# Kernel tuning notes

Measured on AMD Instinct MI355X. Metric: run time of the kernel, lower is better.

Reference implementation:

```python
import jax, jax.numpy as jnp
import numpy as np

V = 33
EPS = 1e-5
PAD = 4  # (temporal_k=9 - 1) // 2
BONES = [(0,1),(1,2),(2,3),(3,7),(0,4),(4,5),(5,6),(6,8),(9,10),(11,12),(11,13),(13,15),(15,17),(15,19),(15,21),(17,19),(12,14),(14,16),(16,18),(16,20),(16,22),(18,20),(11,23),(12,24),(23,24),(23,25),(24,26),(25,27),(26,28),(27,29),(28,30),(29,31),(30,32),(27,31),(28,32)]


def _build_A():
    A = np.zeros((V, V), np.float32)
    for a, b in BONES:
        A[a, b] = 1.0
        A[b, a] = 1.0
    A = A + np.eye(V, dtype=np.float32)
    dis = np.diag(A.sum(1) ** -0.5)
    return jnp.asarray((dis @ A @ dis).astype(np.float32))


def _bn(x, g, b, m, v):
    # inference-mode BatchNorm2d over channel axis 1 of (B,C,T,V)
    inv = g / jnp.sqrt(v + EPS)
    return x * inv[None, :, None, None] + (b - m * inv)[None, :, None, None]


def _block(x, A, pw, pb, g1, b1, m1, v1, tw, tb, g2, b2, m2, v2, rw=None, rb=None):
    # residual branch (1x1 conv if channels change, else identity)
    r = x if rw is None else jnp.einsum('bctv,oc->botv', x, rw) + rb[None, :, None, None]
    # spatial GCN: per-joint 1x1 conv then adjacency mix along joints
    y = jnp.einsum('bctv,oc->botv', x, pw) + pb[None, :, None, None]
    y = jnp.einsum('bctv,vw->bctw', y, A)
    y = jax.nn.relu(_bn(y, g1, b1, m1, v1))
    # temporal conv: kernel (9,1), same padding along T
    y = jax.lax.conv_general_dilated(y, tw, (1, 1), ((PAD, PAD), (0, 0)),
                                     dimension_numbers=('NCHW', 'OIHW', 'NCHW'))
    y = _bn(y + tb[None, :, None, None], g2, b2, m2, v2)
    # Dropout2d is identity in inference mode
    return jax.nn.relu(y + r)


def setup_inputs() -> dict:
    key = jax.random.key(0)
    ks = iter(jax.random.split(key, 80))
    B, C, T, NC = 64, 6, 256, 100
    chans = [6, 32, 64, 64]
    inp = {'x': jax.random.normal(next(ks), (B, C, T, V), jnp.float32),
           'A': _build_A()}

    def add_bn(p, n):
        inp[p + '_g'] = jax.random.uniform(next(ks), (n,), jnp.float32) + 0.5
        inp[p + '_b'] = jax.random.normal(next(ks), (n,), jnp.float32) * 0.1
        inp[p + '_m'] = jax.random.normal(next(ks), (n,), jnp.float32) * 0.1
        inp[p + '_v'] = jax.random.uniform(next(ks), (n,), jnp.float32) + 0.5

    add_bn('bn_in', C * V)
    for i in range(3):
        ci, co = chans[i], chans[i + 1]
        p = 'b%d' % i
        inp[p + '_proj_w'] = jax.random.normal(next(ks), (co, ci), jnp.float32) / np.sqrt(ci).astype(np.float32)
        inp[p + '_proj_b'] = jnp.zeros((co,), jnp.float32)
        add_bn(p + '_bn1', co)
        inp[p + '_tcn_w'] = jax.random.normal(next(ks), (co, co, 9, 1), jnp.float32) / np.sqrt(co * 9).astype(np.float32)
        inp[p + '_tcn_b'] = jnp.zeros((co,), jnp.float32)
        add_bn(p + '_bn2', co)
        if ci != co:
            inp[p + '_res_w'] = jax.random.normal(next(ks), (co, ci), jnp.float32) / np.sqrt(ci).astype(np.float32)
            inp[p + '_res_b'] = jnp.zeros((co,), jnp.float32)
    inp['fc_w'] = jax.random.normal(next(ks), (NC, 64), jnp.float32) * 0.1
    inp['fc_b'] = jnp.zeros((NC,), jnp.float32)
    return inp


def reference(x, A, bn_in_g, bn_in_b, bn_in_m, bn_in_v,
              b0_proj_w, b0_proj_b, b0_bn1_g, b0_bn1_b, b0_bn1_m, b0_bn1_v,
              b0_tcn_w, b0_tcn_b, b0_bn2_g, b0_bn2_b, b0_bn2_m, b0_bn2_v,
              b0_res_w, b0_res_b,
              b1_proj_w, b1_proj_b, b1_bn1_g, b1_bn1_b, b1_bn1_m, b1_bn1_v,
              b1_tcn_w, b1_tcn_b, b1_bn2_g, b1_bn2_b, b1_bn2_m, b1_bn2_v,
              b1_res_w, b1_res_b,
              b2_proj_w, b2_proj_b, b2_bn1_g, b2_bn1_b, b2_bn1_m, b2_bn1_v,
              b2_tcn_w, b2_tcn_b, b2_bn2_g, b2_bn2_b, b2_bn2_m, b2_bn2_v,
              fc_w, fc_b):
    B, C, T, _ = x.shape
    # input BN over C*V channels: torch views as (B, C*V, T) with channel c*V+v
    inv = (bn_in_g / jnp.sqrt(bn_in_v + EPS)).reshape(C, V)
    shift = (bn_in_b - bn_in_m * bn_in_g / jnp.sqrt(bn_in_v + EPS)).reshape(C, V)
    h = x * inv[None, :, None, :] + shift[None, :, None, :]
    h = _block(h, A, b0_proj_w, b0_proj_b, b0_bn1_g, b0_bn1_b, b0_bn1_m, b0_bn1_v,
               b0_tcn_w, b0_tcn_b, b0_bn2_g, b0_bn2_b, b0_bn2_m, b0_bn2_v, b0_res_w, b0_res_b)
    h = _block(h, A, b1_proj_w, b1_proj_b, b1_bn1_g, b1_bn1_b, b1_bn1_m, b1_bn1_v,
               b1_tcn_w, b1_tcn_b, b1_bn2_g, b1_bn2_b, b1_bn2_m, b1_bn2_v, b1_res_w, b1_res_b)
    h = _block(h, A, b2_proj_w, b2_proj_b, b2_bn1_g, b2_bn1_b, b2_bn1_m, b2_bn1_v,
               b2_tcn_w, b2_tcn_b, b2_bn2_g, b2_bn2_b, b2_bn2_m, b2_bn2_v)
    feat = h.mean(axis=(2, 3))  # global avg pool over T, V -> (B, 64)
    return feat @ fc_w.T + fc_b
```

## Files before the change

kernel.cpp:

```cpp
#include <hip/hip_runtime.h>


typedef short bf16s;
using v8s = __attribute__((ext_vector_type(8))) short;
using v4f = __attribute__((ext_vector_type(4))) float;

#define TV 8448
#define NB 64
#define EPSBN 1e-5f

__device__ __forceinline__ float b2f(short s) {
  unsigned u = ((unsigned)(unsigned short)s) << 16;
  return __builtin_bit_cast(float, u);
}
__device__ __forceinline__ short f2b(float f) {
  unsigned u = __builtin_bit_cast(unsigned, f);
  u += 0x7FFFu + ((u >> 16) & 1u);
  return (short)(u >> 16);
}

constexpr int NOFF[34] = {0,3,6,9,12,15,18,21,23,25,27,29,33,37,40,43,48,53,
                          56,59,62,65,67,69,73,77,80,83,87,91,94,97,100,103};
constexpr int NBR[103] = {
  0,1,4,    0,1,2,    1,2,3,    2,3,7,    0,4,5,    4,5,6,    5,6,8,
  3,7,      6,8,      9,10,     9,10,
  11,12,13,23,  11,12,14,24,  11,13,15,  12,14,16,
  13,15,17,19,21,  14,16,18,20,22,
  15,17,19,  16,18,20,  15,17,19,  16,18,20,  15,21,  16,22,
  11,23,24,25,  12,23,24,26,  23,25,27,  24,26,28,
  25,27,29,31,  26,28,30,32,  27,29,31,  28,30,32,  27,29,31,  28,30,32};

constexpr int P_A     = 0;
constexpr int P_INV0  = 1089;
constexpr int P_BIAS0 = 1287;
constexpr int P_PB0   = 1485;
constexpr int P_PB1   = 1517;
constexpr int P_PB2   = 1581;
constexpr int P_I1_0  = 1645;  constexpr int P_B1_0 = 1677;
constexpr int P_I2_0  = 1709;  constexpr int P_B2_0 = 1741;
constexpr int P_I1_1  = 1773;  constexpr int P_B1_1 = 1837;
constexpr int P_I2_1  = 1901;  constexpr int P_B2_1 = 1965;
constexpr int P_I1_2  = 2029;  constexpr int P_B1_2 = 2093;
constexpr int P_I2_2  = 2157;  constexpr int P_B2_2 = 2221;
constexpr int P_FCW   = 2285;
constexpr int P_FCB   = 8685;
constexpr int P_FEAT  = 8785;
constexpr int P_PW0T  = 12881;
constexpr size_t FRAG_OFF = 52480;
constexpr int FRS0 = 1024;
constexpr int FCV0 = 2048;
constexpr int FPJ1 = 11264;
constexpr int FRS1 = 13312;
constexpr int FCV1 = 15360;
constexpr int FPJ2 = 52224;
constexpr int FRS2 = 56320;
constexpr int FCV2 = 60416;
constexpr size_t ACT_OFF = FRAG_OFF + 97280 * 2;
constexpr size_t E64 = (size_t)NB * TV * 64;
constexpr size_t E32 = (size_t)NB * TV * 32;

struct Ptrs { const float* p[48]; };

__device__ void bn1set(int tid, float* inv, float* sh, const float* g,
                       const float* b, const float* m, const float* v, int n) {
  for (int i = tid; i < n; i += 256) {
    float iv = g[i] / sqrtf(v[i] + EPSBN);
    inv[i] = iv; sh[i] = b[i] - m[i] * iv;
  }
}
__device__ void bn2set(int tid, float* inv, float* sh, const float* tb,
                       const float* g, const float* b, const float* m,
                       const float* v, const float* rb, int n) {
  for (int i = tid; i < n; i += 256) {
    float iv = g[i] / sqrtf(v[i] + EPSBN);
    inv[i] = iv;
    sh[i] = tb[i] * iv + b[i] - m[i] * iv + (rb ? rb[i] : 0.f);
  }
}

__device__ void frag_proj(int tid, short* dst, const float* W, int CIr,
                          int KS, int NT) {
  int total = KS * NT * 512;
  for (int idx = tid; idx < total; idx += 256) {
    int s = idx / (NT * 512), r = idx % (NT * 512);
    int nt = r / 512, r2 = r % 512;
    int lane = r2 >> 3, j = r2 & 7;
    int o = nt * 16 + (lane & 15);
    int ci = s * 32 + ((lane >> 4) * 8) + j;
    dst[idx] = f2b((ci < CIr) ? W[o * CIr + ci] : 0.f);
  }
}
__device__ void frag_res(int tid, short* dst, const float* W, int CIr, int ident,
                         const float* g2, const float* v2, int KS, int NT) {
  int total = KS * NT * 512;
  for (int idx = tid; idx < total; idx += 256) {
    int s = idx / (NT * 512), r = idx % (NT * 512);
    int nt = r / 512, r2 = r % 512;
    int lane = r2 >> 3, j = r2 & 7;
    int o = nt * 16 + (lane & 15);
    int ci = s * 32 + ((lane >> 4) * 8) + j;
    float val = 0.f;
    if (ident) { if (ci == o) val = 1.f; }
    else if (ci < CIr) val = W[o * CIr + ci];
    val *= sqrtf(v2[o] + EPSBN) / g2[o];
    dst[idx] = f2b(val);
  }
}
__device__ void frag_conv(int tid, short* dst, const float* tw, int CI, int NT) {
  int total = (CI / 32) * 9 * NT * 512;
  for (int idx = tid; idx < total; idx += 256) {
    int s = idx / (NT * 512), r = idx % (NT * 512);
    int nt = r / 512, r2 = r % 512;
    int lane = r2 >> 3, j = r2 & 7;
    int o = nt * 16 + (lane & 15);
    int kk = ((lane >> 4) * 8) + j;
    int cc = s / 9, tap = s % 9;
    int c = cc * 32 + kk;
    dst[idx] = f2b(tw[(o * CI + c) * 9 + tap]);
  }
}

__global__ __launch_bounds__(256) void prep_kernel(Ptrs in, float* __restrict__ ws,
                                                   short* __restrict__ fr) {
  const int tid = threadIdx.x;
  switch (blockIdx.x) {
    case 0: {
      for (int i = tid; i < 1089; i += 256) ws[P_A + i] = in.p[1][i];
      for (int i = tid; i < 198; i += 256) {
        float iv = in.p[2][i] / sqrtf(in.p[5][i] + EPSBN);
        ws[P_INV0 + i] = iv; ws[P_BIAS0 + i] = in.p[3][i] - in.p[4][i] * iv;
      }
      for (int i = tid; i < 32; i += 256) ws[P_PB0 + i] = in.p[7][i];
      for (int i = tid; i < 64; i += 256) { ws[P_PB1 + i] = in.p[21][i]; ws[P_PB2 + i] = in.p[35][i]; }
      bn1set(tid, ws + P_I1_0, ws + P_B1_0, in.p[8],  in.p[9],  in.p[10], in.p[11], 32);
      bn1set(tid, ws + P_I1_1, ws + P_B1_1, in.p[22], in.p[23], in.p[24], in.p[25], 64);
      bn1set(tid, ws + P_I1_2, ws + P_B1_2, in.p[36], in.p[37], in.p[38], in.p[39], 64);
      bn2set(tid, ws + P_I2_0, ws + P_B2_0, in.p[13], in.p[14], in.p[15], in.p[16], in.p[17], in.p[19], 32);
      bn2set(tid, ws + P_I2_1, ws + P_B2_1, in.p[27], in.p[28], in.p[29], in.p[30], in.p[31], in.p[33], 64);
      bn2set(tid, ws + P_I2_2, ws + P_B2_2, in.p[41], in.p[42], in.p[43], in.p[44], in.p[45], nullptr, 64);
      for (int i = tid; i < 6400; i += 256) ws[P_FCW + i] = in.p[46][i];
      for (int i = tid; i < 100; i += 256) ws[P_FCB + i] = in.p[47][i];
      for (int i = tid; i < 4096; i += 256) ws[P_FEAT + i] = 0.f;
      break;
    }
    case 1: {
      for (int i = tid; i < 192; i += 256) {
        int c = i >> 5, o = i & 31;
        ws[P_PW0T + i] = in.p[6][o * 6 + c];
      }
      break;
    }
    case 2: frag_res (tid, fr + FRS0, in.p[18], 6, 0, in.p[14], in.p[17], 1, 2); break;
    case 3: frag_conv(tid, fr + FCV0, in.p[12], 32, 2); break;
    case 4: frag_proj(tid, fr + FPJ1, in.p[20], 32, 1, 4); break;
    case 5: frag_res (tid, fr + FRS1, in.p[32], 32, 0, in.p[28], in.p[31], 1, 4); break;
    case 6: frag_conv(tid, fr + FCV1, in.p[26], 64, 4); break;
    case 7: frag_proj(tid, fr + FPJ2, in.p[34], 64, 2, 4); break;
    case 8: frag_res (tid, fr + FRS2, nullptr, 0, 1, in.p[42], in.p[45], 2, 4); break;
    case 9: frag_conv(tid, fr + FCV2, in.p[40], 64, 4); break;
  }
}

__global__ __launch_bounds__(256) void pm0_kern(const float* __restrict__ x,
                                                const float* __restrict__ ws,
                                                short* __restrict__ y0,
                                                short* __restrict__ xb) {
  __shared__ __align__(16) short hw[264 * 8];
  const int tid = threadIdx.x;
  const int t0 = blockIdx.x * 8, b = blockIdx.y;
  for (int i = tid; i < 264; i += 256) {
    int tt = i / 33, v = i % 33;
    int t = t0 + tt;
    v8s pack = {0,0,0,0,0,0,0,0};
#pragma unroll
    for (int c = 0; c < 6; c++) {
      float xv = x[((size_t)(b * 6 + c)) * TV + t * 33 + v];
      pack[c] = f2b(fmaf(xv, ws[P_INV0 + c * 33 + v], ws[P_BIAS0 + c * 33 + v]));
    }
    *(v8s*)(hw + (v * 8 + tt) * 8) = pack;
  }
  __syncthreads();
  for (int rr = tid; rr < 264; rr += 256) {
    int v = rr >> 3, tt = rr & 7;
    *(v8s*)(xb + (((size_t)(b * 33 + v)) * 256 + t0 + tt) * 8) =
        *(const v8s*)(hw + rr * 8);
  }
  __syncthreads();
  if (tid < 48) {
    int tt = tid / 6, c = tid % 6;
    float z[33];
#pragma unroll
    for (int v = 0; v < 33; v++) z[v] = b2f(hw[(v * 8 + tt) * 8 + c]);
#pragma unroll
    for (int w = 0; w < 33; w++) {
      float s = 0.f;
#pragma unroll
      for (int j = NOFF[w]; j < NOFF[w + 1]; j++)
        s = fmaf(ws[P_A + w * 33 + NBR[j]], z[NBR[j]], s);
      hw[(w * 8 + tt) * 8 + c] = f2b(s);
    }
  }
  __syncthreads();
  for (int rr = tid; rr < 264; rr += 256) {
    int v = rr >> 3, tt = rr & 7;
    float hv[6];
#pragma unroll
    for (int c = 0; c < 6; c++) hv[c] = b2f(hw[rr * 8 + c]);
    float acc[32];
#pragma unroll
    for (int o = 0; o < 32; o++) acc[o] = ws[P_PB0 + o];
#pragma unroll
    for (int c = 0; c < 6; c++)
#pragma unroll
      for (int o = 0; o < 32; o++) acc[o] = fmaf(hv[c], ws[P_PW0T + c * 32 + o], acc[o]);
    short* dst = y0 + (((size_t)(b * 33 + v)) * 256 + t0 + tt) * 32;
#pragma unroll
    for (int u = 0; u < 4; u++) {
      v8s t;
#pragma unroll
      for (int j = 0; j < 8; j++) {
        int o = u * 8 + j;
        t[j] = f2b(fmaxf(fmaf(acc[o], ws[P_I1_0 + o], ws[P_B1_0 + o]), 0.f));
      }
      *(v8s*)(dst + u * 8) = t;
    }
  }
}

template <int CI>
__global__ __launch_bounds__(256, 4) void pm_kern(const short* __restrict__ in,
                                                  const short* __restrict__ fpj,
                                                  const float* __restrict__ ws,
                                                  short* __restrict__ y,
                                                  int pbO, int i1O, int b1O) {
  constexpr int KS = CI / 32;
  constexpr int RSI = CI + 8;
  constexpr int CH = CI / 8;
  __shared__ __align__(16) short hw[264 * RSI];
  const int tid = threadIdx.x;
  const int t0 = blockIdx.x * 8, b = blockIdx.y;
  const int lane = tid & 63, wv = tid >> 6;
  const int ln = lane & 15, q8 = (lane >> 4) * 8;

  const v8s* pf = (const v8s*)fpj;
  v8s bf[KS][4];
#pragma unroll
  for (int ks = 0; ks < KS; ks++)
#pragma unroll
    for (int nt = 0; nt < 4; nt++) bf[ks][nt] = pf[(ks * 4 + nt) * 64 + lane];

  for (int u = tid; u < 264 * CH; u += 256) {
    int v = u / (8 * CH), r = u % (8 * CH);
    int tt = r / CH, c0 = (r % CH) * 8;
    *(v8s*)(hw + (v * 8 + tt) * RSI + c0) =
        *(const v8s*)(in + (((size_t)(b * 33 + v)) * 256 + t0 + tt) * CI + c0);
  }
  __syncthreads();

  for (int u = tid; u < 8 * CI; u += 256) {
    int tt = u / CI, oc = u % CI;
    float z[33];
#pragma unroll
    for (int v = 0; v < 33; v++) z[v] = b2f(hw[(v * 8 + tt) * RSI + oc]);
#pragma unroll
    for (int w = 0; w < 33; w++) {
      float s = 0.f;
#pragma unroll
      for (int j = NOFF[w]; j < NOFF[w + 1]; j++)
        s = fmaf(ws[P_A + w * 33 + NBR[j]], z[NBR[j]], s);
      hw[(w * 8 + tt) * RSI + oc] = f2b(s);
    }
  }
  __syncthreads();

  for (int i = 0; i < 5; i++) {
    int tile = wv + 4 * i;
    if (tile < 17) {
      int arow = tile * 16 + ln;
      v8s afr[KS];
#pragma unroll
      for (int ks = 0; ks < KS; ks++) {
        v8s zv = {0,0,0,0,0,0,0,0};
        afr[ks] = (arow < 264) ? *(const v8s*)(hw + arow * RSI + ks * 32 + q8) : zv;
      }
      v4f d[4];
#pragma unroll
      for (int nt = 0; nt < 4; nt++) d[nt] = (v4f){0.f, 0.f, 0.f, 0.f};
#pragma unroll
      for (int ks = 0; ks < KS; ks++)
#pragma unroll
        for (int nt = 0; nt < 4; nt++)
          d[nt] = __builtin_amdgcn_mfma_f32_16x16x32_bf16(afr[ks], bf[ks][nt], d[nt], 0, 0, 0);
#pragma unroll
      for (int nt = 0; nt < 4; nt++) {
        int o = nt * 16 + ln;
        float i1 = ws[i1O + o];
        float sh = fmaf(ws[pbO + o], i1, ws[b1O + o]);
#pragma unroll
        for (int r = 0; r < 4; r++) {
          int rr = tile * 16 + (lane >> 4) * 4 + r;
          if (rr < 264) {
            int v = rr >> 3, tt = rr & 7;
            y[(((size_t)(b * 33 + v)) * 256 + t0 + tt) * 64 + o] =
                f2b(fmaxf(fmaf(d[nt][r], i1, sh), 0.f));
          }
        }
      }
    }
  }
}

template <int CI, int CO, int RMODE, bool POOL>
__global__ __launch_bounds__(256, 4) void tcn_kern(
    const short* __restrict__ y, const short* __restrict__ res,
    const short* __restrict__ fcv, const short* __restrict__ frs,
    const float* __restrict__ ws, short* __restrict__ out,
    float* __restrict__ feat, int i2O, int b2O) {
  constexpr int NT = CO / 16;
  constexpr int RSI = CI + 8;
  constexpr int CH = CI / 8;
  constexpr int S = (CI / 32) * 9;
  constexpr int RESOFF = 264 * RSI;
  constexpr int LDSZ = (RMODE == 0) ? (264 * RSI + 2080) : (264 * RSI);
  __shared__ __align__(16) short win[LDSZ];
  const int tid = threadIdx.x;
  const int v = blockIdx.x, b = blockIdx.y;
  const int lane = tid & 63, wv = tid >> 6;
  const int ln = lane & 15, q8 = (lane >> 4) * 8;
  const int wvbase = wv * 64;
  const v8s* cf = (const v8s*)fcv;
  const v8s* rf = (const v8s*)frs;
  const size_t plane = ((size_t)(b * 33 + v)) * 256;

  v8s bcur[NT];
#pragma unroll
  for (int nt = 0; nt < NT; nt++) bcur[nt] = cf[nt * 64 + lane];

  const short* src = y + plane * CI;
  for (int u = tid; u < 264 * CH; u += 256) {
    int r = u / CH, c0 = (u % CH) * 8;
    int t = r - 4;
    v8s val = {0,0,0,0,0,0,0,0};
    if (t >= 0 && t < 256) val = *(const v8s*)(src + (size_t)t * CI + c0);
    *(v8s*)(win + r * RSI + c0) = val;
  }
  if constexpr (RMODE == 0) {
    for (int u = tid; u < 260; u += 256) {
      v8s val = {0,0,0,0,0,0,0,0};
      if (u < 256) val = *(const v8s*)(res + (plane + u) * 8);
      *(v8s*)(win + RESOFF + u * 8) = val;
    }
  }
  __syncthreads();

  v4f acc[4][NT];
#pragma unroll
  for (int mt = 0; mt < 4; mt++)
#pragma unroll
    for (int nt = 0; nt < NT; nt++) acc[mt][nt] = (v4f){0.f, 0.f, 0.f, 0.f};

  for (int s = 0; s < S; s++) {
    int cc = s / 9, tap = s % 9;
    v8s bnx[NT];
    if (s + 1 < S) {
#pragma unroll
      for (int nt = 0; nt < NT; nt++) bnx[nt] = cf[((s + 1) * NT + nt) * 64 + lane];
    }
    v8s afr[4];
#pragma unroll
    for (int mt = 0; mt < 4; mt++) {
      int row = wvbase + mt * 16 + ln + tap;
      afr[mt] = *(const v8s*)(win + row * RSI + cc * 32 + q8);
    }
#pragma unroll
    for (int mt = 0; mt < 4; mt++)
#pragma unroll
      for (int nt = 0; nt < NT; nt++)
        acc[mt][nt] = __builtin_amdgcn_mfma_f32_16x16x32_bf16(
            afr[mt], bcur[nt], acc[mt][nt], 0, 0, 0);
    if (s + 1 < S) {
#pragma unroll
      for (int nt = 0; nt < NT; nt++) bcur[nt] = bnx[nt];
    }
  }

  if constexpr (RMODE == 0) {
    v8s rb[NT];
#pragma unroll
    for (int nt = 0; nt < NT; nt++) rb[nt] = rf[nt * 64 + lane];
    v8s afr[4];
#pragma unroll
    for (int mt = 0; mt < 4; mt++) {
      int row = wvbase + mt * 16 + ln;
      afr[mt] = *(const v8s*)(win + RESOFF + row * 8 + q8);
    }
#pragma unroll
    for (int mt = 0; mt < 4; mt++)
#pragma unroll
      for (int nt = 0; nt < NT; nt++)
        acc[mt][nt] = __builtin_amdgcn_mfma_f32_16x16x32_bf16(
            afr[mt], rb[nt], acc[mt][nt], 0, 0, 0);
  } else {
    constexpr int RKS = (RMODE == 2) ? 2 : 1;
    __syncthreads();
    constexpr int RCH = (RMODE == 2) ? 8 : 4;
    for (int u = tid; u < 256 * RCH; u += 256) {
      int r = u / RCH, c0 = (u % RCH) * 8;
      *(v8s*)(win + r * RSI + c0) =
          *(const v8s*)(res + (plane + r) * (RKS * 32) + c0);
    }
    __syncthreads();
#pragma unroll
    for (int ks = 0; ks < RKS; ks++) {
      v8s rb[NT];
#pragma unroll
      for (int nt = 0; nt < NT; nt++) rb[nt] = rf[(ks * NT + nt) * 64 + lane];
      v8s afr[4];
#pragma unroll
      for (int mt = 0; mt < 4; mt++) {
        int row = wvbase + mt * 16 + ln;
        afr[mt] = *(const v8s*)(win + row * RSI + ks * 32 + q8);
      }
#pragma unroll
      for (int mt = 0; mt < 4; mt++)
#pragma unroll
        for (int nt = 0; nt < NT; nt++)
          acc[mt][nt] = __builtin_amdgcn_mfma_f32_16x16x32_bf16(
              afr[mt], rb[nt], acc[mt][nt], 0, 0, 0);
    }
  }

  if constexpr (POOL) {
    float ps[NT];
#pragma unroll
    for (int nt = 0; nt < NT; nt++) {
      int o = nt * 16 + ln;
      float sA = ws[i2O + o], sB = ws[b2O + o];
      float sl = 0.f;
#pragma unroll
      for (int mt = 0; mt < 4; mt++)
#pragma unroll
        for (int r = 0; r < 4; r++)
          sl += fmaxf(fmaf(acc[mt][nt][r], sA, sB), 0.f);
      ps[nt] = sl;
    }
#pragma unroll
    for (int nt = 0; nt < NT; nt++) {
      ps[nt] += __shfl_xor(ps[nt], 16);
      ps[nt] += __shfl_xor(ps[nt], 32);
    }
    __syncthreads();
    float* pl = (float*)win;
    if (lane < 16) {
#pragma unroll
      for (int nt = 0; nt < NT; nt++) pl[wv * 64 + nt * 16 + lane] = ps[nt];
    }
    __syncthreads();
    if (tid < 64)
      atomicAdd(&feat[b * 64 + tid],
                pl[tid] + pl[64 + tid] + pl[128 + tid] + pl[192 + tid]);
  } else {
#pragma unroll
    for (int nt = 0; nt < NT; nt++) {
      int o = nt * 16 + ln;
      float sA = ws[i2O + o], sB = ws[b2O + o];
#pragma unroll
      for (int mt = 0; mt < 4; mt++)
#pragma unroll
        for (int r = 0; r < 4; r++) {
          int t = wvbase + mt * 16 + (lane >> 4) * 4 + r;
          float val = fmaxf(fmaf(acc[mt][nt][r], sA, sB), 0.f);
          out[(plane + t) * CO + o] = f2b(val);
        }
    }
  }
}

__global__ __launch_bounds__(128) void k4_kern(const float* __restrict__ ws,
                                               float* __restrict__ out) {
  const int b = blockIdx.x, tid = threadIdx.x;
  __shared__ float sf[64];
  if (tid < 64) sf[tid] = ws[P_FEAT + b * 64 + tid] * (1.f / 8448.f);
  __syncthreads();
  if (tid < 100) {
    float a = ws[P_FCB + tid];
#pragma unroll
    for (int o = 0; o < 64; o++) a = fmaf(ws[P_FCW + tid * 64 + o], sf[o], a);
    out[b * 100 + tid] = a;
  }
}

extern "C" void kernel_launch(void* const* d_in, const int* in_sizes, int n_in,
                              void* d_out, int out_size, void* d_ws, size_t ws_size,
                              hipStream_t stream) {
  const float* xin = (const float*)d_in[0];
  float* wsf = (float*)d_ws;
  char* wsb = (char*)d_ws;
  short* frags = (short*)(wsb + FRAG_OFF);
  short* RA = (short*)(wsb + ACT_OFF);
  short* RB = RA + E64;
  short* RC = RB + E64;
  short* y0 = RB;
  short* xb = RB + E32;
  short* h0 = RC;
  short* y1 = RA;
  short* h1 = RB;
  short* y2 = RA;
  float* feat = wsf + P_FEAT;

  Ptrs ptrs;
  for (int i = 0; i < 48 && i < n_in; i++) ptrs.p[i] = (const float*)d_in[i];

  prep_kernel<<<10, 256, 0, stream>>>(ptrs, wsf, frags);

  dim3 gpm(32, NB), gtc(33, NB);
  pm0_kern<<<gpm, 256, 0, stream>>>(xin, wsf, y0, xb);
  tcn_kern<32, 32, 0, false><<<gtc, 256, 0, stream>>>(
      y0, xb, frags + FCV0, frags + FRS0, wsf, h0, nullptr, P_I2_0, P_B2_0);
  pm_kern<32><<<gpm, 256, 0, stream>>>(h0, frags + FPJ1, wsf, y1, P_PB1, P_I1_1, P_B1_1);
  tcn_kern<64, 64, 1, false><<<gtc, 256, 0, stream>>>(
      y1, h0, frags + FCV1, frags + FRS1, wsf, h1, nullptr, P_I2_1, P_B2_1);
  pm_kern<64><<<gpm, 256, 0, stream>>>(h1, frags + FPJ2, wsf, y2, P_PB2, P_I1_2, P_B1_2);
  tcn_kern<64, 64, 2, true><<<gtc, 256, 0, stream>>>(
      y2, h1, frags + FCV2, frags + FRS2, wsf, nullptr, feat, P_I2_2, P_B2_2);
  k4_kern<<<NB, 128, 0, stream>>>(wsf, (float*)d_out);
}
```

Baseline: 387.7 us.

## Stage TCN weight fragments through LDS via async global_load_lds double buffering

Temporal conv weight fragments are now fetched with global_load_lds into a double-buffered LDS staging area, one wave per output tile, and read back from LDS each step. Previously every wave loaded all weight fragments from global memory into registers. This cuts redundant global loads and register pressure, but adds a __syncthreads per tap step. The residual operand for the non-identity residual modes is now read straight from global memory instead of being copied into LDS first, which removes two barriers and a copy loop.

```diff
diff --git a/kernel.cpp b/kernel.cpp
--- a/kernel.cpp
+++ b/kernel.cpp
@@ -17,6 +17,11 @@
   unsigned u = __builtin_bit_cast(unsigned, f);
   u += 0x7FFFu + ((u >> 16) & 1u);
   return (short)(u >> 16);
+}
+__device__ __forceinline__ void gll16(const void* g, void* l) {
+  __builtin_amdgcn_global_load_lds(
+      (const __attribute__((address_space(1))) void*)g,
+      (__attribute__((address_space(3))) void*)l, 16, 0, 0);
 }
 
 constexpr int NOFF[34] = {0,3,6,9,12,15,18,21,23,25,27,29,33,37,40,43,48,53,
@@ -321,20 +326,21 @@
   constexpr int CH = CI / 8;
   constexpr int S = (CI / 32) * 9;
   constexpr int RESOFF = 264 * RSI;
-  constexpr int LDSZ = (RMODE == 0) ? (264 * RSI + 2080) : (264 * RSI);
+  constexpr int BOFF = (RMODE == 0) ? (RESOFF + 2080) : RESOFF;
+  constexpr int BSTEP = NT * 512;
+  constexpr int LDSZ = BOFF + 2 * BSTEP;
   __shared__ __align__(16) short win[LDSZ];
   const int tid = threadIdx.x;
   const int v = blockIdx.x, b = blockIdx.y;
   const int lane = tid & 63, wv = tid >> 6;
   const int ln = lane & 15, q8 = (lane >> 4) * 8;
   const int wvbase = wv * 64;
-  const v8s* cf = (const v8s*)fcv;
   const v8s* rf = (const v8s*)frs;
   const size_t plane = ((size_t)(b * 33 + v)) * 256;
-
-  v8s bcur[NT];
-#pragma unroll
-  for (int nt = 0; nt < NT; nt++) bcur[nt] = cf[nt * 64 + lane];
+  short* bstage = win + BOFF;
+
+  if (NT == 4 || wv < 2)
+    gll16(fcv + ((size_t)wv * 64 + lane) * 8, bstage + wv * 512);
 
   const short* src = y + plane * CI;
   for (int u = tid; u < 264 * CH; u += 256) {
@@ -361,11 +367,13 @@
 
   for (int s = 0; s < S; s++) {
     int cc = s / 9, tap = s % 9;
-    v8s bnx[NT];
-    if (s + 1 < S) {
-#pragma unroll
-      for (int nt = 0; nt < NT; nt++) bnx[nt] = cf[((s + 1) * NT + nt) * 64 + lane];
-    }
+    if (s + 1 < S && (NT == 4 || wv < 2))
+      gll16(fcv + ((size_t)(s + 1) * NT * 64 + wv * 64 + lane) * 8,
+            bstage + ((s + 1) & 1) * BSTEP + wv * 512);
+    v8s bfr[NT];
+#pragma unroll
+    for (int nt = 0; nt < NT; nt++)
+      bfr[nt] = *(const v8s*)(bstage + (s & 1) * BSTEP + (nt * 64 + lane) * 8);
     v8s afr[4];
 #pragma unroll
     for (int mt = 0; mt < 4; mt++) {
@@ -377,11 +385,8 @@
 #pragma unroll
       for (int nt = 0; nt < NT; nt++)
         acc[mt][nt] = __builtin_amdgcn_mfma_f32_16x16x32_bf16(
-            afr[mt], bcur[nt], acc[mt][nt], 0, 0, 0);
-    if (s + 1 < S) {
-#pragma unroll
-      for (int nt = 0; nt < NT; nt++) bcur[nt] = bnx[nt];
-    }
+            afr[mt], bfr[nt], acc[mt][nt], 0, 0, 0);
+    __syncthreads();
   }
 
   if constexpr (RMODE == 0) {
@@ -402,14 +407,7 @@
             afr[mt], rb[nt], acc[mt][nt], 0, 0, 0);
   } else {
     constexpr int RKS = (RMODE == 2) ? 2 : 1;
-    __syncthreads();
-    constexpr int RCH = (RMODE == 2) ? 8 : 4;
-    for (int u = tid; u < 256 * RCH; u += 256) {
-      int r = u / RCH, c0 = (u % RCH) * 8;
-      *(v8s*)(win + r * RSI + c0) =
-          *(const v8s*)(res + (plane + r) * (RKS * 32) + c0);
-    }
-    __syncthreads();
+    constexpr int RST = RKS * 32;
 #pragma unroll
     for (int ks = 0; ks < RKS; ks++) {
       v8s rb[NT];
@@ -419,7 +417,7 @@
 #pragma unroll
       for (int mt = 0; mt < 4; mt++) {
         int row = wvbase + mt * 16 + ln;
-        afr[mt] = *(const v8s*)(win + row * RSI + ks * 32 + q8);
+        afr[mt] = *(const v8s*)(res + (plane + row) * RST + ks * 32 + q8);
       }
 #pragma unroll
       for (int mt = 0; mt < 4; mt++)
```

Result: faster. 375.5 us (-3.2%).
